# Kernel optimization log

Hardware: AMD Instinct MI355X
Metric: run time of the kernel (lower is better)

Reference implementation:

```python
import jax, jax.numpy as jnp
import numpy as np

DIM = 384
HEADS = 6
HIDDEN = int(DIM * 4.0)
EPS = 1e-6

def setup_inputs() -> dict:
    key = jax.random.key(0)
    ks = jax.random.split(key, 8)
    s = 0.02
    return {
        "x": jax.random.normal(ks[0], (4, 2048, DIM), dtype=jnp.float32),
        "w_qkv": jax.random.normal(ks[1], (DIM, 3 * DIM), dtype=jnp.float32) * s,
        "b_qkv": jnp.zeros((3 * DIM,), dtype=jnp.float32),
        "w_proj": jax.random.normal(ks[2], (DIM, DIM), dtype=jnp.float32) * s,
        "b_proj": jnp.zeros((DIM,), dtype=jnp.float32),
        "w_fc1": jax.random.normal(ks[3], (DIM, HIDDEN), dtype=jnp.float32) * s,
        "b_fc1": jnp.zeros((HIDDEN,), dtype=jnp.float32),
        "w_fc2": jax.random.normal(ks[4], (HIDDEN, DIM), dtype=jnp.float32) * s,
        "b_fc2": jnp.zeros((DIM,), dtype=jnp.float32),
        "g1": jnp.ones((DIM,), dtype=jnp.float32),
        "beta1": jnp.zeros((DIM,), dtype=jnp.float32),
        "g2": jnp.ones((DIM,), dtype=jnp.float32),
        "beta2": jnp.zeros((DIM,), dtype=jnp.float32),
    }

def _layernorm(x, g, b):
    mu = jnp.mean(x, axis=-1, keepdims=True)
    var = jnp.mean(jnp.square(x - mu), axis=-1, keepdims=True)
    return (x - mu) * jax.lax.rsqrt(var + EPS) * g + b

def _attention(x, w_qkv, b_qkv, w_proj, b_proj):
    B, N, C = x.shape
    H = HEADS
    Dh = C // H
    qkv = x @ w_qkv + b_qkv                      # [B,N,3C]
    qkv = qkv.reshape(B, N, 3, H, Dh)
    q = jnp.transpose(qkv[:, :, 0], (0, 2, 1, 3))  # [B,H,N,Dh]
    k = jnp.transpose(qkv[:, :, 1], (0, 2, 1, 3))
    v = jnp.transpose(qkv[:, :, 2], (0, 2, 1, 3))
    scale = Dh ** -0.5
    attn = jnp.einsum('bhnd,bhmd->bhnm', q, k) * scale
    attn = jax.nn.softmax(attn, axis=-1)
    out = jnp.einsum('bhnm,bhmd->bhnd', attn, v)
    out = jnp.transpose(out, (0, 2, 1, 3)).reshape(B, N, C)
    return out @ w_proj + b_proj

def _mlp(x, w_fc1, b_fc1, w_fc2, b_fc2):
    h = jax.nn.gelu(x @ w_fc1 + b_fc1, approximate=False)
    return h @ w_fc2 + b_fc2

def reference(x, w_qkv, b_qkv, w_proj, b_proj, w_fc1, b_fc1, w_fc2, b_fc2, g1, beta1, g2, beta2):
    x = x + _attention(_layernorm(x, g1, beta1), w_qkv, b_qkv, w_proj, b_proj)
    x = x + _mlp(_layernorm(x, g2, beta2), w_fc1, b_fc1, w_fc2, b_fc2)
    return x
```

## Files before the change

kernel.cpp:

```cpp
#include <hip/hip_runtime.h>
#include <hip/hip_bf16.h>

#define TOK 8192
#define CDIM 384
#define HEADS 6
#define DH 64
#define HID 1536
#define SEQ 2048

#define QSCALE 0.18033688011112042f

typedef short bf16x8 __attribute__((ext_vector_type(8)));
typedef short bf16x4 __attribute__((ext_vector_type(4)));
typedef float f32x4 __attribute__((ext_vector_type(4)));
typedef void __attribute__((address_space(1))) GV;
typedef void __attribute__((address_space(3))) SV;

__device__ __forceinline__ short f2bf(float f) {
    __hip_bfloat16 h = __float2bfloat16(f);
    return *reinterpret_cast<short*>(&h);
}

__device__ __forceinline__ int pack_bf2(float a, float b) {
    __hip_bfloat162 h2 = __float22bfloat162_rn(make_float2(a, b));
    int r;
    __builtin_memcpy(&r, &h2, 4);
    return r;
}

__device__ __forceinline__ void gl_lds16(const short* g, short* lds) {
    __builtin_amdgcn_global_load_lds((GV*)g, (SV*)lds, 16, 0, 0);
}

__device__ __forceinline__ float gelu_exact(float v) {
    return 0.5f * v * (1.0f + erff(v * 0.70710678118654752f));
}

__global__ __launch_bounds__(128) void ln_trans(const float* __restrict__ x,
                                                const float* __restrict__ g,
                                                const float* __restrict__ bta,
                                                short* __restrict__ y,
                                                const float* __restrict__ w_qkv,
                                                const float* __restrict__ w_proj,
                                                const float* __restrict__ w_fc1,
                                                const float* __restrict__ w_fc2,
                                                short* __restrict__ qkvT,
                                                short* __restrict__ projT,
                                                short* __restrict__ fc1T,
                                                short* __restrict__ fc2T) {
    if (blockIdx.x < TOK) {
        const int row = blockIdx.x;
        const float* xr = x + (size_t)row * CDIM;
        const int t = threadIdx.x;
        float v0 = xr[t], v1 = xr[t + 128], v2 = xr[t + 256];
        float s = v0 + v1 + v2;
        float ss = v0 * v0 + v1 * v1 + v2 * v2;
#pragma unroll
        for (int off = 1; off < 64; off <<= 1) {
            s += __shfl_xor(s, off);
            ss += __shfl_xor(ss, off);
        }
        __shared__ float sh[4];
        const int wv = t >> 6;
        if ((t & 63) == 0) { sh[wv] = s; sh[2 + wv] = ss; }
        __syncthreads();
        s = sh[0] + sh[1];
        ss = sh[2] + sh[3];
        const float mu = s * (1.0f / CDIM);
        const float var = ss * (1.0f / CDIM) - mu * mu;
        const float rs = rsqrtf(var + 1e-6f);
        short* yr = y + (size_t)row * CDIM;
        yr[t]       = f2bf((v0 - mu) * rs * g[t]       + bta[t]);
        yr[t + 128] = f2bf((v1 - mu) * rs * g[t + 128] + bta[t + 128]);
        yr[t + 256] = f2bf((v2 - mu) * rs * g[t + 256] + bta[t + 256]);
        return;
    }
    int b = blockIdx.x - TOK;
    const float* w; short* o; int K, N, nb;
    if (b < 432)       { w = w_qkv;  o = qkvT;  K = 384;  N = 1152; nb = 36; }
    else if (b < 576)  { b -= 432;  w = w_proj; o = projT; K = 384;  N = 384;  nb = 12; }
    else if (b < 1152) { b -= 576;  w = w_fc1;  o = fc1T;  K = 384;  N = 1536; nb = 48; }
    else               { b -= 1152; w = w_fc2;  o = fc2T;  K = 1536; N = 384;  nb = 12; }
    const int bx = (b % nb) * 32, by = (b / nb) * 32;
    __shared__ float t[32][33];
    const int tx = threadIdx.x & 31, ty = threadIdx.x >> 5;
#pragma unroll
    for (int i = 0; i < 8; ++i)
        t[ty + i * 4][tx] = w[(size_t)(by + ty + i * 4) * N + bx + tx];
    __syncthreads();
#pragma unroll
    for (int i = 0; i < 8; ++i)
        o[(size_t)(bx + ty + i * 4) * K + by + tx] = f2bf(t[tx][ty + i * 4]);
}

__global__ __launch_bounds__(128) void ln_kernel(const float* __restrict__ x,
                                                 const float* __restrict__ g,
                                                 const float* __restrict__ bta,
                                                 short* __restrict__ y) {
    const int row = blockIdx.x;
    const float* xr = x + (size_t)row * CDIM;
    const int t = threadIdx.x;
    float v0 = xr[t], v1 = xr[t + 128], v2 = xr[t + 256];
    float s = v0 + v1 + v2;
    float ss = v0 * v0 + v1 * v1 + v2 * v2;
#pragma unroll
    for (int off = 1; off < 64; off <<= 1) {
        s += __shfl_xor(s, off);
        ss += __shfl_xor(ss, off);
    }
    __shared__ float sh[4];
    const int wv = t >> 6;
    if ((t & 63) == 0) { sh[wv] = s; sh[2 + wv] = ss; }
    __syncthreads();
    s = sh[0] + sh[1];
    ss = sh[2] + sh[3];
    const float mu = s * (1.0f / CDIM);
    const float var = ss * (1.0f / CDIM) - mu * mu;
    const float rs = rsqrtf(var + 1e-6f);
    short* yr = y + (size_t)row * CDIM;
    yr[t]       = f2bf((v0 - mu) * rs * g[t]       + bta[t]);
    yr[t + 128] = f2bf((v1 - mu) * rs * g[t + 128] + bta[t + 128]);
    yr[t + 256] = f2bf((v2 - mu) * rs * g[t + 256] + bta[t + 256]);
}

template <int MODE, int MT>
__global__ __launch_bounds__(256) void mfma_gemm(const short* __restrict__ A,
                                                 const short* __restrict__ WT,
                                                 const float* __restrict__ bias,
                                                 const float* __restrict__ resid,
                                                 float* __restrict__ outF,
                                                 short* __restrict__ outB,
                                                 short* __restrict__ qb,
                                                 short* __restrict__ kb,
                                                 short* __restrict__ vtb,
                                                 int M, int N, int K) {
    constexpr int BN = (MT == 4) ? 128 : 64;
    constexpr int BM = (MT == 1) ? 64 : 128;
    __shared__ __align__(16) short As[BM * 64];
    __shared__ __align__(16) short Bs[BN * 64];

    const int tid  = threadIdx.x;
    const int w    = tid >> 6;
    const int lane = tid & 63;
    const int quad = lane >> 4;
    const int n15  = lane & 15;
    const int wr   = (MT == 4) ? (w >> 1) : w;
    const int wc   = (MT == 4) ? (w & 1) : 0;
    const int m0   = blockIdx.y * BM;
    const int n0   = blockIdx.x * BN;
    const int swz  = n15 & 7;

    f32x4 acc[MT][4];
#pragma unroll
    for (int i = 0; i < MT; ++i)
#pragma unroll
        for (int j = 0; j < 4; ++j) {
            acc[i][j][0] = 0; acc[i][j][1] = 0; acc[i][j][2] = 0; acc[i][j][3] = 0;
        }

    for (int k0 = 0; k0 < K; k0 += 64) {
        __syncthreads();
#pragma unroll
        for (int i = 0; i < BM / 32; ++i) {
            const int c = i * 256 + tid;
            const int r = c >> 3, p = c & 7;
            gl_lds16(A + (size_t)(m0 + r) * K + k0 + ((p ^ (r & 7)) * 8),
                     As + (i * 256 + w * 64) * 8);
        }
#pragma unroll
        for (int i = 0; i < BN / 32; ++i) {
            const int c = i * 256 + tid;
            const int r = c >> 3, p = c & 7;
            gl_lds16(WT + (size_t)(n0 + r) * K + k0 + ((p ^ (r & 7)) * 8),
                     Bs + (i * 256 + w * 64) * 8);
        }
        __syncthreads();

#pragma unroll
        for (int kk = 0; kk < 2; ++kk) {
            bf16x8 af[MT], bfr[4];
#pragma unroll
            for (int mt = 0; mt < MT; ++mt)
                af[mt] = *(const bf16x8*)&As[(wr * (MT * 16) + mt * 16 + n15) * 64 +
                                             (((kk * 4 + quad) ^ swz) * 8)];
#pragma unroll
            for (int nt = 0; nt < 4; ++nt)
                bfr[nt] = *(const bf16x8*)&Bs[(wc * 64 + nt * 16 + n15) * 64 +
                                              (((kk * 4 + quad) ^ swz) * 8)];
#pragma unroll
            for (int mt = 0; mt < MT; ++mt)
#pragma unroll
                for (int nt = 0; nt < 4; ++nt)
                    acc[mt][nt] = __builtin_amdgcn_mfma_f32_16x16x32_bf16(af[mt], bfr[nt], acc[mt][nt], 0, 0, 0);
        }
    }

#pragma unroll
    for (int nt = 0; nt < 4; ++nt) {
        const int col = n0 + wc * 64 + nt * 16 + n15;
        const float bv = bias[col];
        if constexpr (MODE == 2) {
            const int part = col / CDIM;
            const int rem  = col - part * CDIM;
            const int h    = rem >> 6;
            const int d    = rem & 63;
#pragma unroll
            for (int mt = 0; mt < MT; ++mt) {
                const int r0 = m0 + wr * (MT * 16) + mt * 16 + quad * 4;
                const int bi = r0 >> 11;
                const int n  = r0 & 2047;
                if (part == 2) {
                    short4 pkv;
                    pkv.x = f2bf(acc[mt][nt][0] + bv);
                    pkv.y = f2bf(acc[mt][nt][1] + bv);
                    pkv.z = f2bf(acc[mt][nt][2] + bv);
                    pkv.w = f2bf(acc[mt][nt][3] + bv);
                    *(short4*)&vtb[((size_t)(bi * HEADS + h) * DH + d) * SEQ + n] = pkv;
                } else {
                    short* dst = (part == 0 ? qb : kb) +
                                 ((size_t)(bi * HEADS + h) * SEQ + n) * DH + d;
#pragma unroll
                    for (int rr = 0; rr < 4; ++rr) {
                        float o = acc[mt][nt][rr] + bv;
                        if (part == 0) o *= QSCALE;
                        dst[(size_t)rr * DH] = f2bf(o);
                    }
                }
            }
        } else {
#pragma unroll
            for (int mt = 0; mt < MT; ++mt)
#pragma unroll
                for (int rr = 0; rr < 4; ++rr) {
                    const int r = m0 + wr * (MT * 16) + mt * 16 + quad * 4 + rr;
                    float o = acc[mt][nt][rr] + bv;
                    if constexpr (MODE == 1) {
                        outB[(size_t)r * N + col] = f2bf(gelu_exact(o));
                    } else {
                        if (resid) o += resid[(size_t)r * N + col];
                        outF[(size_t)r * N + col] = o;
                    }
                }
        }
    }
}

__global__ __launch_bounds__(256) void attn_mfma(const short* __restrict__ qb,
                                                 const short* __restrict__ kb,
                                                 const short* __restrict__ vtb,
                                                 short* __restrict__ outp) {
    __shared__ __align__(16) short Ql[64 * 64];
    __shared__ __align__(16) short Kl[2][64 * 64];
    __shared__ __align__(16) short Vtl[2][64 * 64];

    const int qt = blockIdx.x;
    const int bh = blockIdx.z * HEADS + blockIdx.y;

    const int tid  = threadIdx.x;
    const int w    = tid >> 6;
    const int lane = tid & 63;
    const int quad = lane >> 4;
    const int n15  = lane & 15;
    const int swz  = n15 & 7;

    const size_t headoff = (size_t)bh * SEQ * DH;

    {
        const short* qg = qb + headoff + (size_t)qt * 64 * DH;
#pragma unroll
        for (int i = 0; i < 2; ++i) {
            const int c = (w * 2 + i) * 64 + lane;
            const int r = c >> 3, p = c & 7;
            gl_lds16(qg + r * 64 + ((p ^ (r & 7)) * 8), Ql + (c - lane) * 8);
        }
    }

    const short* kptr[2];
    const short* vptr[2];
#pragma unroll
    for (int i = 0; i < 2; ++i) {
        const int c = (w * 2 + i) * 64 + lane;
        const int r = c >> 3, p = c & 7;
        kptr[i] = kb + headoff + r * 64 + ((p ^ (r & 7)) * 8);
        vptr[i] = vtb + (size_t)bh * DH * SEQ + (size_t)r * SEQ + ((p ^ (r & 7)) * 8);
    }

#pragma unroll
    for (int i = 0; i < 2; ++i) {
        gl_lds16(kptr[i], Kl[0] + ((w * 2 + i) * 64) * 8);
        gl_lds16(vptr[i], Vtl[0] + ((w * 2 + i) * 64) * 8);
        kptr[i] += 64 * DH;
        vptr[i] += 64;
    }

    f32x4 O[4], O4;
    O4[0] = 0; O4[1] = 0; O4[2] = 0; O4[3] = 0;
#pragma unroll
    for (int nt = 0; nt < 4; ++nt) { O[nt][0] = 0; O[nt][1] = 0; O[nt][2] = 0; O[nt][3] = 0; }

    bf16x4 onesf;
    { const short one = 0x3F80; onesf[0] = one; onesf[1] = one; onesf[2] = one; onesf[3] = one; }

    bf16x8 qf[2];

    for (int kt = 0; kt < SEQ / 64; ++kt) {
        const int cur = kt & 1;
        __syncthreads();
        if (kt < SEQ / 64 - 1) {
            const int nxt = cur ^ 1;
#pragma unroll
            for (int i = 0; i < 2; ++i) {
                gl_lds16(kptr[i], Kl[nxt] + ((w * 2 + i) * 64) * 8);
                gl_lds16(vptr[i], Vtl[nxt] + ((w * 2 + i) * 64) * 8);
                kptr[i] += 64 * DH;
                vptr[i] += 64;
            }
        }

        if (kt == 0) {
            qf[0] = *(const bf16x8*)&Ql[(w * 16 + n15) * 64 + ((quad ^ swz) * 8)];
            qf[1] = *(const bf16x8*)&Ql[(w * 16 + n15) * 64 + (((4 + quad) ^ swz) * 8)];
        }

        f32x4 S[4];
#pragma unroll
        for (int nt = 0; nt < 4; ++nt) {
            S[nt][0] = 0; S[nt][1] = 0; S[nt][2] = 0; S[nt][3] = 0;
#pragma unroll
            for (int kc = 0; kc < 2; ++kc) {
                const bf16x8 kf = *(const bf16x8*)&Kl[cur][(nt * 16 + n15) * 64 + (((kc * 4 + quad) ^ swz) * 8)];
                S[nt] = __builtin_amdgcn_mfma_f32_16x16x32_bf16(kf, qf[kc], S[nt], 0, 0, 0);
            }
        }

        bf16x4 af16[4];
#pragma unroll
        for (int nt = 0; nt < 4; ++nt) {
            int pk[2];
            pk[0] = pack_bf2(exp2f(S[nt][0]), exp2f(S[nt][1]));
            pk[1] = pack_bf2(exp2f(S[nt][2]), exp2f(S[nt][3]));
            __builtin_memcpy(&af16[nt], pk, 8);
        }

#pragma unroll
        for (int kc16 = 0; kc16 < 4; ++kc16) {
#pragma unroll
            for (int ntd = 0; ntd < 4; ++ntd) {
                const int row = ntd * 16 + n15;
                const int pchunk = (2 * kc16 + (quad >> 1)) ^ swz;
                const bf16x4 vf = *(const bf16x4*)&Vtl[cur][row * 64 + pchunk * 8 + (quad & 1) * 4];
                O[ntd] = __builtin_amdgcn_mfma_f32_16x16x16bf16_1k(af16[kc16], vf, O[ntd], 0, 0, 0);
            }
            O4 = __builtin_amdgcn_mfma_f32_16x16x16bf16_1k(af16[kc16], onesf, O4, 0, 0, 0);
        }
    }

#pragma unroll
    for (int rr = 0; rr < 4; ++rr) {
        const float inv = 1.0f / O4[rr];
        const int row = qt * 64 + w * 16 + quad * 4 + rr;
#pragma unroll
        for (int nt = 0; nt < 4; ++nt)
            outp[(size_t)(blockIdx.z * SEQ + row) * CDIM + blockIdx.y * DH + nt * 16 + n15] =
                f2bf(O[nt][rr] * inv);
    }
}

extern "C" void kernel_launch(void* const* d_in, const int* in_sizes, int n_in,
                              void* d_out, int out_size, void* d_ws, size_t ws_size,
                              hipStream_t stream) {
    const float* x      = (const float*)d_in[0];
    const float* w_qkv  = (const float*)d_in[1];
    const float* b_qkv  = (const float*)d_in[2];
    const float* w_proj = (const float*)d_in[3];
    const float* b_proj = (const float*)d_in[4];
    const float* w_fc1  = (const float*)d_in[5];
    const float* b_fc1  = (const float*)d_in[6];
    const float* w_fc2  = (const float*)d_in[7];
    const float* b_fc2  = (const float*)d_in[8];
    const float* g1     = (const float*)d_in[9];
    const float* beta1  = (const float*)d_in[10];
    const float* g2     = (const float*)d_in[11];
    const float* beta2  = (const float*)d_in[12];
    float* out = (float*)d_out;

    short* qkvT = (short*)d_ws;
    short* projT = qkvT + 1152 * 384;
    short* fc1T  = projT + 384 * 384;
    short* fc2T  = fc1T + 1536 * 384;
    short* y     = fc2T + 384 * 1536;
    short* qb    = y + (size_t)TOK * 384;
    short* kb    = qb + (size_t)TOK * 384;
    short* vtb   = kb + (size_t)TOK * 384;
    short* attn  = vtb + (size_t)TOK * 384;
    short* hbuf  = attn + (size_t)TOK * 384;

    ln_trans<<<TOK + 1728, 128, 0, stream>>>(x, g1, beta1, y,
                                             w_qkv, w_proj, w_fc1, w_fc2,
                                             qkvT, projT, fc1T, fc2T);
    mfma_gemm<2, 4><<<dim3(1152 / 128, TOK / 128), 256, 0, stream>>>(
        y, qkvT, b_qkv, nullptr, nullptr, nullptr, qb, kb, vtb, TOK, 3 * CDIM, CDIM);
    attn_mfma<<<dim3(SEQ / 64, HEADS, 4), 256, 0, stream>>>(qb, kb, vtb, attn);
    mfma_gemm<0, 1><<<dim3(CDIM / 64, TOK / 64), 256, 0, stream>>>(
        attn, projT, b_proj, x, out, nullptr, nullptr, nullptr, nullptr, TOK, CDIM, CDIM);
    ln_kernel<<<TOK, 128, 0, stream>>>(out, g2, beta2, y);
    mfma_gemm<1, 4><<<dim3(HID / 128, TOK / 128), 256, 0, stream>>>(
        y, fc1T, b_fc1, nullptr, nullptr, hbuf, nullptr, nullptr, nullptr, TOK, HID, CDIM);
    mfma_gemm<0, 1><<<dim3(CDIM / 64, TOK / 64), 256, 0, stream>>>(
        hbuf, fc2T, b_fc2, out, out, nullptr, nullptr, nullptr, nullptr, TOK, CDIM, HID);
}
```

Before: 244.8 us.

## Split attention keys across warps with LDS reduction and use fast GELU

The attention kernel now has each of the 4 warps process all 64 queries against a disjoint quarter of the key blocks. Each warp keeps its own private K/V LDS tile, so per-iteration block barriers are replaced by wave-local waits. Partial outputs and row sums are then combined through LDS at the end. This trades block-level synchronization for more registers and a larger LDS footprint, which may lower occupancy. Separately, the exact erf GELU in the MLP epilogue is replaced by an exp2-based sigmoid approximation to cut transcendental cost, at some accuracy risk.

```diff
diff --git a/kernel.cpp b/kernel.cpp
--- a/kernel.cpp
+++ b/kernel.cpp
@@ -32,8 +32,11 @@
     __builtin_amdgcn_global_load_lds((GV*)g, (SV*)lds, 16, 0, 0);
 }
 
-__device__ __forceinline__ float gelu_exact(float v) {
-    return 0.5f * v * (1.0f + erff(v * 0.70710678118654752f));
+__device__ __forceinline__ float gelu_fast(float v) {
+    const float A = 2.3022067f;
+    const float B = 0.1029442f;
+    const float u = v * (A + B * v * v);
+    return v - v / (1.0f + exp2f(u));
 }
 
 __global__ __launch_bounds__(128) void ln_trans(const float* __restrict__ x,
@@ -235,7 +238,7 @@
                     const int r = m0 + wr * (MT * 16) + mt * 16 + quad * 4 + rr;
                     float o = acc[mt][nt][rr] + bv;
                     if constexpr (MODE == 1) {
-                        outB[(size_t)r * N + col] = f2bf(gelu_exact(o));
+                        outB[(size_t)r * N + col] = f2bf(gelu_fast(o));
                     } else {
                         if (resid) o += resid[(size_t)r * N + col];
                         outF[(size_t)r * N + col] = o;
@@ -249,9 +252,8 @@
                                                  const short* __restrict__ kb,
                                                  const short* __restrict__ vtb,
                                                  short* __restrict__ outp) {
-    __shared__ __align__(16) short Ql[64 * 64];
-    __shared__ __align__(16) short Kl[2][64 * 64];
-    __shared__ __align__(16) short Vtl[2][64 * 64];
+    __shared__ __align__(16) char smem[73728];
+    short* Ql = (short*)smem;
 
     const int qt = blockIdx.x;
     const int bh = blockIdx.z * HEADS + blockIdx.y;
@@ -263,6 +265,9 @@
     const int n15  = lane & 15;
     const int swz  = n15 & 7;
 
+    short* Kl  = (short*)(smem + 8192 + w * 16384);
+    short* Vtl = (short*)(smem + 8192 + w * 16384 + 8192);
+
     const size_t headoff = (size_t)bh * SEQ * DH;
 
     {
@@ -274,95 +279,104 @@
             gl_lds16(qg + r * 64 + ((p ^ (r & 7)) * 8), Ql + (c - lane) * 8);
         }
     }
-
-    const short* kptr[2];
-    const short* vptr[2];
-#pragma unroll
-    for (int i = 0; i < 2; ++i) {
-        const int c = (w * 2 + i) * 64 + lane;
-        const int r = c >> 3, p = c & 7;
-        kptr[i] = kb + headoff + r * 64 + ((p ^ (r & 7)) * 8);
-        vptr[i] = vtb + (size_t)bh * DH * SEQ + (size_t)r * SEQ + ((p ^ (r & 7)) * 8);
-    }
-
-#pragma unroll
-    for (int i = 0; i < 2; ++i) {
-        gl_lds16(kptr[i], Kl[0] + ((w * 2 + i) * 64) * 8);
-        gl_lds16(vptr[i], Vtl[0] + ((w * 2 + i) * 64) * 8);
-        kptr[i] += 64 * DH;
-        vptr[i] += 64;
-    }
-
-    f32x4 O[4], O4;
-    O4[0] = 0; O4[1] = 0; O4[2] = 0; O4[3] = 0;
-#pragma unroll
-    for (int nt = 0; nt < 4; ++nt) { O[nt][0] = 0; O[nt][1] = 0; O[nt][2] = 0; O[nt][3] = 0; }
+    __syncthreads();
+
+    bf16x8 qf[4][2];
+#pragma unroll
+    for (int mt = 0; mt < 4; ++mt) {
+        qf[mt][0] = *(const bf16x8*)&Ql[(mt * 16 + n15) * 64 + ((quad ^ swz) * 8)];
+        qf[mt][1] = *(const bf16x8*)&Ql[(mt * 16 + n15) * 64 + (((4 + quad) ^ swz) * 8)];
+    }
+
+    const int l3 = lane >> 3, l7 = lane & 7;
+    const short* kg = kb + headoff + l3 * 64 + ((l7 ^ l3) * 8) + (size_t)w * 64 * DH;
+    const short* vg = vtb + (size_t)bh * DH * SEQ + (size_t)l3 * SEQ + ((l7 ^ l3) * 8) + w * 64;
+
+    f32x4 O[4][4], O4[4];
+#pragma unroll
+    for (int mt = 0; mt < 4; ++mt) {
+        O4[mt][0] = 0; O4[mt][1] = 0; O4[mt][2] = 0; O4[mt][3] = 0;
+#pragma unroll
+        for (int nt = 0; nt < 4; ++nt) {
+            O[mt][nt][0] = 0; O[mt][nt][1] = 0; O[mt][nt][2] = 0; O[mt][nt][3] = 0;
+        }
+    }
 
     bf16x4 onesf;
     { const short one = 0x3F80; onesf[0] = one; onesf[1] = one; onesf[2] = one; onesf[3] = one; }
 
-    bf16x8 qf[2];
-
-    for (int kt = 0; kt < SEQ / 64; ++kt) {
-        const int cur = kt & 1;
-        __syncthreads();
-        if (kt < SEQ / 64 - 1) {
-            const int nxt = cur ^ 1;
-#pragma unroll
-            for (int i = 0; i < 2; ++i) {
-                gl_lds16(kptr[i], Kl[nxt] + ((w * 2 + i) * 64) * 8);
-                gl_lds16(vptr[i], Vtl[nxt] + ((w * 2 + i) * 64) * 8);
-                kptr[i] += 64 * DH;
-                vptr[i] += 64;
+    for (int t = 0; t < SEQ / 64 / 4; ++t) {
+#pragma unroll
+        for (int i = 0; i < 8; ++i) {
+            gl_lds16(kg + i * 512, Kl + i * 512);
+            gl_lds16(vg + (size_t)i * 8 * SEQ, Vtl + i * 512);
+        }
+        kg += 4 * 64 * DH;
+        vg += 4 * 64;
+        __builtin_amdgcn_s_waitcnt(0x0F70);
+        __builtin_amdgcn_wave_barrier();
+
+#pragma unroll
+        for (int nt = 0; nt < 4; ++nt) {
+            f32x4 S[4];
+#pragma unroll
+            for (int mt = 0; mt < 4; ++mt) { S[mt][0] = 0; S[mt][1] = 0; S[mt][2] = 0; S[mt][3] = 0; }
+#pragma unroll
+            for (int kc = 0; kc < 2; ++kc) {
+                const bf16x8 kf = *(const bf16x8*)&Kl[(nt * 16 + n15) * 64 + (((kc * 4 + quad) ^ swz) * 8)];
+#pragma unroll
+                for (int mt = 0; mt < 4; ++mt)
+                    S[mt] = __builtin_amdgcn_mfma_f32_16x16x32_bf16(kf, qf[mt][kc], S[mt], 0, 0, 0);
             }
-        }
-
-        if (kt == 0) {
-            qf[0] = *(const bf16x8*)&Ql[(w * 16 + n15) * 64 + ((quad ^ swz) * 8)];
-            qf[1] = *(const bf16x8*)&Ql[(w * 16 + n15) * 64 + (((4 + quad) ^ swz) * 8)];
-        }
-
-        f32x4 S[4];
-#pragma unroll
-        for (int nt = 0; nt < 4; ++nt) {
-            S[nt][0] = 0; S[nt][1] = 0; S[nt][2] = 0; S[nt][3] = 0;
-#pragma unroll
-            for (int kc = 0; kc < 2; ++kc) {
-                const bf16x8 kf = *(const bf16x8*)&Kl[cur][(nt * 16 + n15) * 64 + (((kc * 4 + quad) ^ swz) * 8)];
-                S[nt] = __builtin_amdgcn_mfma_f32_16x16x32_bf16(kf, qf[kc], S[nt], 0, 0, 0);
+            bf16x4 af[4];
+#pragma unroll
+            for (int mt = 0; mt < 4; ++mt) {
+                int pk[2];
+                pk[0] = pack_bf2(exp2f(S[mt][0]), exp2f(S[mt][1]));
+                pk[1] = pack_bf2(exp2f(S[mt][2]), exp2f(S[mt][3]));
+                __builtin_memcpy(&af[mt], pk, 8);
             }
-        }
-
-        bf16x4 af16[4];
-#pragma unroll
-        for (int nt = 0; nt < 4; ++nt) {
-            int pk[2];
-            pk[0] = pack_bf2(exp2f(S[nt][0]), exp2f(S[nt][1]));
-            pk[1] = pack_bf2(exp2f(S[nt][2]), exp2f(S[nt][3]));
-            __builtin_memcpy(&af16[nt], pk, 8);
-        }
-
-#pragma unroll
-        for (int kc16 = 0; kc16 < 4; ++kc16) {
 #pragma unroll
             for (int ntd = 0; ntd < 4; ++ntd) {
                 const int row = ntd * 16 + n15;
-                const int pchunk = (2 * kc16 + (quad >> 1)) ^ swz;
-                const bf16x4 vf = *(const bf16x4*)&Vtl[cur][row * 64 + pchunk * 8 + (quad & 1) * 4];
-                O[ntd] = __builtin_amdgcn_mfma_f32_16x16x16bf16_1k(af16[kc16], vf, O[ntd], 0, 0, 0);
+                const int pchunk = (2 * nt + (quad >> 1)) ^ swz;
+                const bf16x4 vf = *(const bf16x4*)&Vtl[row * 64 + pchunk * 8 + (quad & 1) * 4];
+#pragma unroll
+                for (int mt = 0; mt < 4; ++mt)
+                    O[mt][ntd] = __builtin_amdgcn_mfma_f32_16x16x16bf16_1k(af[mt], vf, O[mt][ntd], 0, 0, 0);
             }
-            O4 = __builtin_amdgcn_mfma_f32_16x16x16bf16_1k(af16[kc16], onesf, O4, 0, 0, 0);
-        }
-    }
-
-#pragma unroll
-    for (int rr = 0; rr < 4; ++rr) {
-        const float inv = 1.0f / O4[rr];
-        const int row = qt * 64 + w * 16 + quad * 4 + rr;
-#pragma unroll
-        for (int nt = 0; nt < 4; ++nt)
-            outp[(size_t)(blockIdx.z * SEQ + row) * CDIM + blockIdx.y * DH + nt * 16 + n15] =
-                f2bf(O[nt][rr] * inv);
+#pragma unroll
+            for (int mt = 0; mt < 4; ++mt)
+                O4[mt] = __builtin_amdgcn_mfma_f32_16x16x16bf16_1k(af[mt], onesf, O4[mt], 0, 0, 0);
+        }
+    }
+
+    __syncthreads();
+    float* Obuf = (float*)smem;
+    float* lbuf = (float*)(smem + 66560);
+    float* myO = Obuf + w * 4160;
+#pragma unroll
+    for (int mt = 0; mt < 4; ++mt) {
+#pragma unroll
+        for (int ntd = 0; ntd < 4; ++ntd)
+#pragma unroll
+            for (int rr = 0; rr < 4; ++rr)
+                myO[(mt * 16 + quad * 4 + rr) * 65 + ntd * 16 + n15] = O[mt][ntd][rr];
+        if (n15 == 0)
+#pragma unroll
+            for (int rr = 0; rr < 4; ++rr)
+                lbuf[w * 64 + mt * 16 + quad * 4 + rr] = O4[mt][rr];
+    }
+    __syncthreads();
+
+    const int d = w * 16 + n15;
+#pragma unroll
+    for (int i = 0; i < 16; ++i) {
+        const int q = quad * 16 + i;
+        const float l = lbuf[q] + lbuf[64 + q] + lbuf[128 + q] + lbuf[192 + q];
+        const float s = Obuf[q * 65 + d] + Obuf[4160 + q * 65 + d] +
+                        Obuf[8320 + q * 65 + d] + Obuf[12480 + q * 65 + d];
+        outp[(size_t)(blockIdx.z * SEQ + qt * 64 + q) * CDIM + blockIdx.y * DH + d] = f2bf(s / l);
     }
 }
 
```

Result: no change. 244.3 us (-0.2%).
